# Optimization experiments

Hardware: AMD Instinct MI355X
Metric: run time of the kernel (lower is better)

Reference implementation:

```python
import jax, jax.numpy as jnp
import numpy as np

B, S, D, H, HD, NF, NL, V = 16, 2048, 768, 12, 64, 32, 12, 2362
EPS = 1e-6  # fast_transformers LinearAttention eps


def _rope_tables(seq_len, dim):
    inv_freq = 1.0 / (10000.0 ** (jnp.arange(0, dim, 2, dtype=jnp.float32) / dim))
    t = jnp.arange(seq_len, dtype=jnp.float32)
    freqs = jnp.einsum('s,f->sf', t, inv_freq)
    emb = jnp.concatenate([freqs, freqs], axis=-1)[None, :, None, :]  # [1,S,1,HD]
    return jnp.cos(emb), jnp.sin(emb)


def _rot_half(x):
    x1, x2 = jnp.split(x, 2, axis=-1)
    return jnp.concatenate([-x2, x1], axis=-1)


def _ln(x, g, b):
    m = jnp.mean(x, axis=-1, keepdims=True)
    v = jnp.var(x, axis=-1, keepdims=True)
    return (x - m) / jnp.sqrt(v + 1e-5) * g + b


def setup_inputs():
    key = jax.random.key(0)
    ks = jax.random.split(key, 16)
    w = lambda k, shape: jax.random.normal(k, shape, jnp.float32) * 0.02
    return {
        'idx': jax.random.randint(ks[0], (B, S), 0, V),
        'mask': jnp.ones((B, S), jnp.int32),
        'emb': w(ks[1], (V, D)),
        'wq': w(ks[2], (NL, D, D)), 'bq': jnp.zeros((NL, D), jnp.float32),
        'wk': w(ks[3], (NL, D, D)), 'bk': jnp.zeros((NL, D), jnp.float32),
        'wv': w(ks[4], (NL, D, D)), 'bv': jnp.zeros((NL, D), jnp.float32),
        'wo': w(ks[5], (NL, D, D)), 'bo': jnp.zeros((NL, D), jnp.float32),
        'omega': jax.random.normal(ks[6], (NL, HD, NF), jnp.float32),
        'g1': jnp.ones((NL, D), jnp.float32), 'be1': jnp.zeros((NL, D), jnp.float32),
        'w1': w(ks[7], (NL, D, D)), 'c1': jnp.zeros((NL, D), jnp.float32),
        'w2': w(ks[8], (NL, D, D)), 'c2': jnp.zeros((NL, D), jnp.float32),
        'g2': jnp.ones((NL, D), jnp.float32), 'be2': jnp.zeros((NL, D), jnp.float32),
        'gf': jnp.ones((D,), jnp.float32), 'bf': jnp.zeros((D,), jnp.float32),
    }


def reference(idx, mask, emb, wq, bq, wk, bk, wv, bv, wo, bo, omega,
              g1, be1, w1, c1, w2, c2, g2, be2, gf, bf):
    x = emb[idx]                     # token embedding [B,S,D]; dropout = identity (eval)
    m = mask.astype(x.dtype)         # LengthMask from mask.sum(-1); mask is contiguous ones
    cos, sin = _rope_tables(S, HD)
    for l in range(NL):
        q = (x @ wq[l] + bq[l]).reshape(B, S, H, HD)
        k = (x @ wk[l] + bk[l]).reshape(B, S, H, HD)
        v = (x @ wv[l] + bv[l]).reshape(B, S, H, HD)
        q = q * cos + _rot_half(q) * sin
        k = k * cos + _rot_half(k) * sin
        # GeneralizedRandomFeatures: phi(x) = relu(x @ omega)
        Qf = jax.nn.relu(jnp.einsum('bshd,df->bshf', q, omega[l]))
        Kf = jax.nn.relu(jnp.einsum('bshd,df->bshf', k, omega[l])) * m[:, :, None, None]
        KV = jnp.einsum('bshf,bshd->bhfd', Kf, v)                       # [B,H,NF,HD]
        Z = 1.0 / (jnp.einsum('bshf,bhf->bsh', Qf, Kf.sum(axis=1)) + EPS)
        a = jnp.einsum('bshf,bhfd,bsh->bshd', Qf, KV, Z).reshape(B, S, D)
        x = x + (a @ wo[l] + bo[l])           # residual (dropout=identity)
        x = _ln(x, g1[l], be1[l])             # post-norm
        y = jax.nn.gelu(x @ w1[l] + c1[l], approximate=False) @ w2[l] + c2[l]
        x = _ln(x + y, g2[l], be2[l])
    return _ln(x, gf, bf)                     # final encoder LayerNorm
```

## Files before the change

### kernel.cpp

```cpp
#include <hip/hip_runtime.h>
#include <cstdint>
#include <cstddef>

typedef __bf16 bf16;
typedef __bf16 bf16x8 __attribute__((ext_vector_type(8)));
typedef __bf16 bf16x4 __attribute__((ext_vector_type(4)));
typedef float f32x4 __attribute__((ext_vector_type(4)));

#define NB 16
#define SS 2048
#define HH 12
#define NLL 12
#define MTOK (NB*SS)

#define BARRIER() do { asm volatile("" ::: "memory"); __builtin_amdgcn_s_barrier(); asm volatile("" ::: "memory"); } while (0)
#define VMCNT0()  asm volatile("s_waitcnt vmcnt(0)" ::: "memory")

__device__ __forceinline__ void load16_lds(const bf16* g, bf16* l) {
    __builtin_amdgcn_global_load_lds((const __attribute__((address_space(1))) void*)g,
                                     (__attribute__((address_space(3))) void*)l, 16, 0, 0);
}

__global__ void diag_k(float* out, float code) {
    if (threadIdx.x == 0 && blockIdx.x == 0) out[0] = code;
}

__global__ __launch_bounds__(256) void packw_k(const float* __restrict__ wq, const float* __restrict__ wk,
                                               const float* __restrict__ wv, const float* __restrict__ wo,
                                               const float* __restrict__ w1, const float* __restrict__ w2,
                                               int l, bf16* qkvT_l, bf16* oT_l, bf16* w1T_l, bf16* w2T_l) {
    __shared__ float tile[32][33];
    int which = blockIdx.z;
    const float* srcs[6] = {wq, wk, wv, wo, w1, w2};
    const float* src = srcs[which] + (size_t)l * 589824;
    bf16* dst;
    if (which < 3)       dst = qkvT_l + (size_t)which * 589824;
    else if (which == 3) dst = oT_l;
    else if (which == 4) dst = w1T_l;
    else                 dst = w2T_l;
    int tx = threadIdx.x, ty = threadIdx.y;
    int bx = blockIdx.x, by = blockIdx.y;
#pragma unroll
    for (int j = 0; j < 4; ++j)
        tile[ty + j*8][tx] = src[(size_t)(by*32 + ty + j*8) * 768 + bx*32 + tx];
    __syncthreads();
#pragma unroll
    for (int j = 0; j < 4; ++j)
        dst[(size_t)(bx*32 + ty + j*8) * 768 + by*32 + tx] = (bf16)tile[tx][ty + j*8];
}

__global__ void packb_k(const float* __restrict__ bq, const float* __restrict__ bk,
                        const float* __restrict__ bv, float* bqkv) {
    int i = blockIdx.x * 256 + threadIdx.x;
    if (i >= NLL * 2304) return;
    int l = i / 2304, c = i % 2304;
    float v = (c < 768) ? bq[l*768 + c] : (c < 1536) ? bk[l*768 + c - 768] : bv[l*768 + c - 1536];
    bqkv[i] = v;
}

__global__ void rope_k(float* cosT, float* sinT) {
    int i = blockIdx.x * 256 + threadIdx.x;
    int s = i >> 6, j = i & 63, f = j & 31;
    float inv = powf(10000.f, -(float)(2*f) * (1.0f/64.0f));
    float ang = (float)s * inv;
    cosT[i] = cosf(ang);
    sinT[i] = sinf(ang);
}

__global__ __launch_bounds__(192) void embed_k(const int* __restrict__ idx, const float* __restrict__ emb,
                                               float* __restrict__ x, bf16* __restrict__ xb) {
    size_t tok = blockIdx.x;
    int t = threadIdx.x;
    int id = idx[tok];
    float4 v = *(const float4*)&emb[(size_t)id * 768 + t*4];
    *(float4*)&x[tok * 768 + t*4] = v;
    bf16x4 o; o[0] = (bf16)v.x; o[1] = (bf16)v.y; o[2] = (bf16)v.z; o[3] = (bf16)v.w;
    *(bf16x4*)&xb[tok * 768 + t*4] = o;
}

__global__ __launch_bounds__(512, 2)
void gemm256_k(const bf16* __restrict__ A, const bf16* __restrict__ Bt,
               const float* __restrict__ bias, bf16* __restrict__ outb, int N) {
    const int K = 768;
    __shared__ bf16 As[2][16384];
    __shared__ bf16 Bs[2][16384];
    const int t = threadIdx.x;
    const int w = t >> 6, lane = t & 63;
    const int wr = w >> 2, wc = w & 3;

    const int nx = gridDim.x;
    const int L = blockIdx.y * nx + blockIdx.x;
    const int xcd = L & 7, bi = L >> 3;
    const int bcol = (bi % nx) * 256;
    const int brow = ((bi / nx) * 8 + xcd) * 256;

    const int srow0 = t >> 3;
    const int scb   = (t & 7) * 16;
    const int scbs  = scb ^ ((srow0 & 7) << 4);
    const int scol  = scbs >> 1;

    auto stageA = [&](int s, int k0, int hh) {
        const bf16* g0 = A + (size_t)(brow + hh*128 + srow0)      * K + k0 + scol;
        const bf16* g1 = A + (size_t)(brow + hh*128 + srow0 + 64) * K + k0 + scol;
        load16_lds(g0, &As[s][hh*8192 + t*8]);
        load16_lds(g1, &As[s][hh*8192 + t*8 + 4096]);
    };
    auto stageB = [&](int s, int k0, int hh) {
        const bf16* g0 = Bt + (size_t)(bcol + hh*128 + srow0)      * K + k0 + scol;
        const bf16* g1 = Bt + (size_t)(bcol + hh*128 + srow0 + 64) * K + k0 + scol;
        load16_lds(g0, &Bs[s][hh*8192 + t*8]);
        load16_lds(g1, &Bs[s][hh*8192 + t*8 + 4096]);
    };

    const int rowa = lane & 15, kg = lane >> 4;
    const int rsw  = (rowa & 7) << 4;

    f32x4  acc[8][4] = {};
    bf16x8 af[4][2];
    bf16x8 bg[2][2][2];

#define LOADAF(CUR, MH)                                                          \
    _Pragma("unroll") for (int mi2 = 0; mi2 < 4; ++mi2)                          \
    _Pragma("unroll") for (int ks = 0; ks < 2; ++ks) {                           \
        int lrow = wr*128 + (MH)*64 + mi2*16 + rowa;                             \
        int cbyt = (ks*64 + kg*16) ^ rsw;                                        \
        af[mi2][ks] = *(const bf16x8*)&As[CUR][lrow*64 + (cbyt >> 1)];           \
    }
#define LOADBG(CUR, NH)                                                          \
    _Pragma("unroll") for (int ni2 = 0; ni2 < 2; ++ni2)                          \
    _Pragma("unroll") for (int ks = 0; ks < 2; ++ks) {                           \
        int lrow = wc*64 + (NH)*32 + ni2*16 + rowa;                              \
        int cbyt = (ks*64 + kg*16) ^ rsw;                                        \
        bg[NH][ni2][ks] = *(const bf16x8*)&Bs[CUR][lrow*64 + (cbyt >> 1)];       \
    }
#define MFMAQ(MH, NH)                                                            \
    __builtin_amdgcn_s_setprio(1);                                               \
    _Pragma("unroll") for (int mi2 = 0; mi2 < 4; ++mi2)                          \
    _Pragma("unroll") for (int ni2 = 0; ni2 < 2; ++ni2)                          \
    _Pragma("unroll") for (int ks = 0; ks < 2; ++ks)                             \
        acc[(MH)*4+mi2][(NH)*2+ni2] = __builtin_amdgcn_mfma_f32_16x16x32_bf16(   \
            af[mi2][ks], bg[NH][ni2][ks], acc[(MH)*4+mi2][(NH)*2+ni2], 0, 0, 0); \
    __builtin_amdgcn_s_setprio(0);

    stageA(0, 0, 0); stageA(0, 0, 1); stageB(0, 0, 0); stageB(0, 0, 1);
    VMCNT0();
    BARRIER();

    for (int kt = 0; kt < 12; ++kt) {
        const int cur = kt & 1, nb = cur ^ 1;
        const int kn = (kt + 1) * 64;
        const bool st = (kt < 11);
        LOADAF(cur, 0);
        LOADBG(cur, 0);
        if (st) { stageA(nb, kn, 0); stageA(nb, kn, 1); }
        BARRIER();
        MFMAQ(0, 0);
        BARRIER();
        LOADBG(cur, 1);
        if (st) stageB(nb, kn, 0);
        BARRIER();
        MFMAQ(0, 1);
        BARRIER();
        LOADAF(cur, 1);
        if (st) stageB(nb, kn, 1);
        BARRIER();
        MFMAQ(1, 1);
        BARRIER();
        MFMAQ(1, 0);
        VMCNT0();
        BARRIER();
    }
#undef LOADAF
#undef LOADBG
#undef MFMAQ

    bf16* Cs = &As[0][0];
    const int r0 = (lane >> 4) * 4, c0 = lane & 15;
    const int ch = t & 15, rr = t >> 4;
#pragma unroll
    for (int h = 0; h < 2; ++h) {
        __syncthreads();
        if ((wc >> 1) == h) {
            const int lc0 = (wc & 1) * 64;
#pragma unroll
            for (int mi = 0; mi < 8; ++mi)
#pragma unroll
                for (int ni = 0; ni < 4; ++ni) {
                    int col = bcol + wc * 64 + ni * 16 + c0;
                    float bv = bias[col];
#pragma unroll
                    for (int r = 0; r < 4; ++r)
                        Cs[(wr*128 + mi*16 + r0 + r) * 128 + lc0 + ni*16 + c0] =
                            (bf16)(acc[mi][ni][r] + bv);
                }
        }
        __syncthreads();
#pragma unroll
        for (int i = 0; i < 8; ++i) {
            int row = rr + i * 32;
            *(bf16x8*)&outb[(size_t)(brow + row) * N + bcol + h*128 + ch*8] =
                *(const bf16x8*)&Cs[row * 128 + ch * 8];
        }
    }
}

template <int MODE>
__global__ __launch_bounds__(256)
void gemm128_k(const bf16* __restrict__ A, const bf16* __restrict__ Bt,
               const float* __restrict__ bias, bf16* __restrict__ outb, int N) {
    const int K = 768;
    __shared__ bf16 sh[16384];
    bf16* As = sh;
    bf16* Bs = sh + 8192;
    const int t = threadIdx.x;
    const int w = t >> 6, lane = t & 63;
    const int wr = w >> 1, wc = w & 1;

    const int nx = gridDim.x;
    const int L = blockIdx.y * nx + blockIdx.x;
    const int xcd = L & 7, bi = L >> 3;
    const int bcol = (bi % nx) * 128;
    const int brow = ((bi / nx) * 8 + xcd) * 128;

    const int srow = t >> 3;
    const int scol = (((t & 7) * 16) ^ ((srow & 7) << 4)) >> 1;
    const int rowa = lane & 15, kg = lane >> 4;
    const int rsw  = (rowa & 7) << 4;

    f32x4 acc[4][4] = {};

    for (int k0 = 0; k0 < K; k0 += 64) {
        __syncthreads();
#pragma unroll
        for (int j = 0; j < 4; ++j) {
            load16_lds(A  + (size_t)(brow + j*32 + srow) * K + k0 + scol, &As[j*2048 + t*8]);
            load16_lds(Bt + (size_t)(bcol + j*32 + srow) * K + k0 + scol, &Bs[j*2048 + t*8]);
        }
        __syncthreads();
        bf16x8 af[4][2], bg[4][2];
#pragma unroll
        for (int mi = 0; mi < 4; ++mi)
#pragma unroll
            for (int ks = 0; ks < 2; ++ks)
                af[mi][ks] = *(const bf16x8*)&As[(wr*64 + mi*16 + rowa)*64 + (((ks*64 + kg*16) ^ rsw) >> 1)];
#pragma unroll
        for (int ni = 0; ni < 4; ++ni)
#pragma unroll
            for (int ks = 0; ks < 2; ++ks)
                bg[ni][ks] = *(const bf16x8*)&Bs[(wc*64 + ni*16 + rowa)*64 + (((ks*64 + kg*16) ^ rsw) >> 1)];
#pragma unroll
        for (int mi = 0; mi < 4; ++mi)
#pragma unroll
            for (int ni = 0; ni < 4; ++ni)
#pragma unroll
                for (int ks = 0; ks < 2; ++ks)
                    acc[mi][ni] = __builtin_amdgcn_mfma_f32_16x16x32_bf16(af[mi][ks], bg[ni][ks], acc[mi][ni], 0, 0, 0);
    }

    __syncthreads();
    const int r0 = (lane >> 4) * 4, c0 = lane & 15;
#pragma unroll
    for (int mi = 0; mi < 4; ++mi)
#pragma unroll
        for (int ni = 0; ni < 4; ++ni) {
            int col = bcol + wc * 64 + ni * 16 + c0;
            float bv = bias[col];
#pragma unroll
            for (int r = 0; r < 4; ++r) {
                float v = acc[mi][ni][r] + bv;
                if (MODE == 1) v = 0.5f * v * (1.f + erff(v * 0.70710678118f));
                sh[(wr*64 + mi*16 + r0 + r) * 128 + wc*64 + ni*16 + c0] = (bf16)v;
            }
        }
    __syncthreads();
    const int ch = t & 15, rr = t >> 4;
#pragma unroll
    for (int i = 0; i < 8; ++i) {
        int row = rr + i * 16;
        *(bf16x8*)&outb[(size_t)(brow + row) * N + bcol + ch*8] =
            *(const bf16x8*)&sh[row * 128 + ch * 8];
    }
}

__global__ __launch_bounds__(192) void phi_k(const bf16* __restrict__ qkv, const float* __restrict__ cosT,
                                             const float* __restrict__ sinT, const float* __restrict__ omega_l,
                                             const int* __restrict__ mask, bf16* __restrict__ Qf,
                                             bf16* __restrict__ Kf) {
    __shared__ float roped[2][4][12][65];
    __shared__ float om[64][32];
    int t = threadIdx.x;
    size_t tok0 = (size_t)blockIdx.x * 4;

    for (int i = t; i < 2048; i += 192) ((float*)om)[i] = omega_l[i];

    {
        int side = t / 96, cr = t % 96, h = cr >> 3, cq = cr & 7;
        float sgn = (cq < 4) ? -1.f : 1.f;
        for (int it = 0; it < 4; ++it) {
            size_t tokg = tok0 + it;
            int s = (int)(tokg & (SS - 1));
            const bf16* rowp = qkv + tokg * 2304 + side * 768 + h * 64;
            bf16x8 mv = *(const bf16x8*)(rowp + cq * 8);
            bf16x8 pv = *(const bf16x8*)(rowp + (cq ^ 4) * 8);
            const float* cp = cosT + s * 64 + cq * 8;
            const float* sp = sinT + s * 64 + cq * 8;
#pragma unroll
            for (int e = 0; e < 8; ++e) {
                float r = (float)mv[e] * cp[e] + sgn * (float)pv[e] * sp[e];
                roped[side][it][h][cq * 8 + e] = r;
            }
        }
    }
    __syncthreads();

    int side = t / 96, rr = t % 96, h = rr >> 3, f0 = (rr & 7) * 4;
    float acc[4][4] = {};
    for (int d = 0; d < 64; ++d) {
        float4 o = *(const float4*)&om[d][f0];
#pragma unroll
        for (int tk = 0; tk < 4; ++tk) {
            float qv = roped[side][tk][h][d];
            acc[tk][0] += qv * o.x; acc[tk][1] += qv * o.y;
            acc[tk][2] += qv * o.z; acc[tk][3] += qv * o.w;
        }
    }
    bf16* outb = (side == 0) ? Qf : Kf;
#pragma unroll
    for (int tk = 0; tk < 4; ++tk) {
        size_t tokg = tok0 + tk;
        float m = (side == 1) ? (float)mask[tokg] : 1.f;
        bf16x4 v;
        v[0] = (bf16)(fmaxf(acc[tk][0], 0.f) * m);
        v[1] = (bf16)(fmaxf(acc[tk][1], 0.f) * m);
        v[2] = (bf16)(fmaxf(acc[tk][2], 0.f) * m);
        v[3] = (bf16)(fmaxf(acc[tk][3], 0.f) * m);
        *(bf16x4*)&outb[(tokg * 12 + h) * 32 + f0] = v;
    }
}

__global__ __launch_bounds__(256) void kvp_k(const bf16* __restrict__ Kf, const bf16* __restrict__ qkv,
                                             float* __restrict__ KVp, float* __restrict__ Ksp) {
    int ch = blockIdx.x, h = blockIdx.y, b = blockIdx.z;
    __shared__ float kts[64][32];
    __shared__ bf16 vts[64][64];
    int t = threadIdx.x;
    int fg = t & 15, dg = t >> 4;
    int f0 = fg * 2, d0 = dg * 4;
    float acc[8] = {};
    float ksm[2] = {};
    for (int s0 = ch * 256; s0 < ch * 256 + 256; s0 += 64) {
        __syncthreads();
        {
            int row = t >> 2, slot = t & 3;
            bf16x8 k8 = *(const bf16x8*)&Kf[((size_t)(b * SS + s0 + row) * 12 + h) * 32 + slot * 8];
#pragma unroll
            for (int e = 0; e < 8; ++e) kts[row][slot * 8 + e] = (float)k8[e];
            int c0 = t, c1 = t + 256;
            *(float4*)&vts[c0 >> 3][(c0 & 7) * 8] =
                *(const float4*)&qkv[(size_t)(b * SS + s0 + (c0 >> 3)) * 2304 + 1536 + h * 64 + (c0 & 7) * 8];
            *(float4*)&vts[c1 >> 3][(c1 & 7) * 8] =
                *(const float4*)&qkv[(size_t)(b * SS + s0 + (c1 >> 3)) * 2304 + 1536 + h * 64 + (c1 & 7) * 8];
        }
        __syncthreads();
#pragma unroll 4
        for (int sl = 0; sl < 64; ++sl) {
            float2 kk = *(const float2*)&kts[sl][f0];
            bf16x4 vv = *(const bf16x4*)&vts[sl][d0];
            float v0 = (float)vv[0], v1 = (float)vv[1], v2 = (float)vv[2], v3 = (float)vv[3];
            acc[0] += kk.x * v0; acc[1] += kk.x * v1; acc[2] += kk.x * v2; acc[3] += kk.x * v3;
            acc[4] += kk.y * v0; acc[5] += kk.y * v1; acc[6] += kk.y * v2; acc[7] += kk.y * v3;
            if (dg == 0) { ksm[0] += kk.x; ksm[1] += kk.y; }
        }
    }
    size_t base = (((size_t)(b * 12 + h) * 8 + ch) * 32) * 64;
#pragma unroll
    for (int i = 0; i < 2; ++i)
#pragma unroll
        for (int j = 0; j < 4; ++j)
            KVp[base + (size_t)(f0 + i) * 64 + d0 + j] = acc[i * 4 + j];
    if (dg == 0) {
        size_t kb = ((size_t)(b * 12 + h) * 8 + ch) * 32;
        Ksp[kb + f0] = ksm[0]; Ksp[kb + f0 + 1] = ksm[1];
    }
}

__global__ __launch_bounds__(256) void kvc_k(const float* __restrict__ KVp, const float* __restrict__ Ksp,
                                             float* __restrict__ KV, float* __restrict__ Ksum) {
    int bh = blockIdx.x, t = threadIdx.x;
    size_t base = (size_t)bh * 8 * 2048;
    float v[8] = {};
    for (int ch = 0; ch < 8; ++ch)
#pragma unroll
        for (int j = 0; j < 8; ++j) v[j] += KVp[base + (size_t)ch * 2048 + t * 8 + j];
#pragma unroll
    for (int j = 0; j < 8; ++j) KV[(size_t)bh * 2048 + t * 8 + j] = v[j];
    if (t < 32) {
        float s = 0.f;
        for (int ch = 0; ch < 8; ++ch) s += Ksp[((size_t)bh * 8 + ch) * 32 + t];
        Ksum[(size_t)bh * 32 + t] = s;
    }
}

__global__ __launch_bounds__(256) void comb_k(const bf16* __restrict__ Qf, const float* __restrict__ KV,
                                              const float* __restrict__ Ksum, bf16* __restrict__ aout) {
    int ch = blockIdx.x, h = blockIdx.y, b = blockIdx.z;
    int bh = b * 12 + h;
    int t = threadIdx.x, sl = t >> 6, d = t & 63;
    const float* kvb = KV + (size_t)bh * 2048;
    const float* ksb = Ksum + (size_t)bh * 32;
    float kvcol[32], ksr[32];
#pragma unroll
    for (int f = 0; f < 32; ++f) kvcol[f] = kvb[f * 64 + d];
#pragma unroll
    for (int f = 0; f < 32; ++f) ksr[f] = ksb[f];
    for (int g = 0; g < 16; ++g) {
        int s = ch * 64 + g * 4 + sl;
        size_t tok = (size_t)b * SS + s;
        const bf16* qf = Qf + (tok * 12 + h) * 32;
        float accd = 0.f, accz = 0.f;
#pragma unroll
        for (int fb = 0; fb < 4; ++fb) {
            bf16x8 q8 = *(const bf16x8*)(qf + fb * 8);
#pragma unroll
            for (int e = 0; e < 8; ++e) {
                float q = (float)q8[e];
                accd += q * kvcol[fb * 8 + e];
                accz += q * ksr[fb * 8 + e];
            }
        }
        float z = 1.f / (accz + 1e-6f);
        aout[tok * 768 + h * 64 + d] = (bf16)(accd * z);
    }
}

__global__ __launch_bounds__(192) void ln2_k(const float* xsrc, const bf16* ysrc,
                                             const float* __restrict__ g, const float* __restrict__ be,
                                             float* xout, bf16* xbout) {
    size_t tok = blockIdx.x;
    int t = threadIdx.x;
    float4 v = *(const float4*)&xsrc[tok * 768 + t * 4];
    if (ysrc) {
        bf16x4 yv = *(const bf16x4*)&ysrc[tok * 768 + t * 4];
        v.x += (float)yv[0]; v.y += (float)yv[1]; v.z += (float)yv[2]; v.w += (float)yv[3];
    }
    float s = v.x + v.y + v.z + v.w;
    float q = v.x * v.x + v.y * v.y + v.z * v.z + v.w * v.w;
#pragma unroll
    for (int off = 32; off > 0; off >>= 1) { s += __shfl_down(s, off); q += __shfl_down(q, off); }
    __shared__ float sred[3], qred[3];
    int w = t >> 6, lane = t & 63;
    if (lane == 0) { sred[w] = s; qred[w] = q; }
    __syncthreads();
    s = sred[0] + sred[1] + sred[2];
    q = qred[0] + qred[1] + qred[2];
    float mean = s * (1.f / 768.f);
    float var = q * (1.f / 768.f) - mean * mean;
    float inv = rsqrtf(var + 1e-5f);
    float4 gg = *(const float4*)&g[t * 4];
    float4 bb = *(const float4*)&be[t * 4];
    float4 o;
    o.x = (v.x - mean) * inv * gg.x + bb.x;
    o.y = (v.y - mean) * inv * gg.y + bb.y;
    o.z = (v.z - mean) * inv * gg.z + bb.z;
    o.w = (v.w - mean) * inv * gg.w + bb.w;
    *(float4*)&xout[tok * 768 + t * 4] = o;
    if (xbout) {
        bf16x4 ob; ob[0] = (bf16)o.x; ob[1] = (bf16)o.y; ob[2] = (bf16)o.z; ob[3] = (bf16)o.w;
        *(bf16x4*)&xbout[tok * 768 + t * 4] = ob;
    }
}

extern "C" void kernel_launch(void* const* d_in, const int* in_sizes, int n_in,
                              void* d_out, int out_size, void* d_ws, size_t ws_size,
                              hipStream_t stream) {
    const int*   idx   = (const int*)d_in[0];
    const int*   mask  = (const int*)d_in[1];
    const float* emb   = (const float*)d_in[2];
    const float* wq    = (const float*)d_in[3];
    const float* bq    = (const float*)d_in[4];
    const float* wk    = (const float*)d_in[5];
    const float* bk    = (const float*)d_in[6];
    const float* wv    = (const float*)d_in[7];
    const float* bv    = (const float*)d_in[8];
    const float* wo    = (const float*)d_in[9];
    const float* bo    = (const float*)d_in[10];
    const float* omega = (const float*)d_in[11];
    const float* g1    = (const float*)d_in[12];
    const float* be1   = (const float*)d_in[13];
    const float* w1    = (const float*)d_in[14];
    const float* c1    = (const float*)d_in[15];
    const float* w2    = (const float*)d_in[16];
    const float* c2    = (const float*)d_in[17];
    const float* g2    = (const float*)d_in[18];
    const float* be2   = (const float*)d_in[19];
    const float* gf    = (const float*)d_in[20];
    const float* bff   = (const float*)d_in[21];
    float* dout = (float*)d_out;

    char* wsb = (char*)d_ws;
    size_t off = 0;
    auto nxt = [&](size_t bytes) -> void* {
        void* p = wsb + off;
        off += bytes;
        off = (off + 255) & ~(size_t)255;
        return p;
    };

    float* cosT  = (float*)nxt((size_t)SS * 64 * 4);
    float* sinT  = (float*)nxt((size_t)SS * 64 * 4);
    bf16*  qkvTl = (bf16*)nxt((size_t)2304 * 768 * 2);
    bf16*  oTl   = (bf16*)nxt((size_t)768 * 768 * 2);
    bf16*  w1Tl  = (bf16*)nxt((size_t)768 * 768 * 2);
    bf16*  w2Tl  = (bf16*)nxt((size_t)768 * 768 * 2);
    float* bqkv  = (float*)nxt((size_t)NLL * 2304 * 4);
    float* x     = (float*)nxt((size_t)MTOK * 768 * 4);
    bf16*  xb    = (bf16*)nxt((size_t)MTOK * 768 * 2);
    bf16*  qkv   = (bf16*)nxt((size_t)MTOK * 2304 * 2);
    bf16*  Qf    = (bf16*)nxt((size_t)MTOK * 384 * 2);
    bf16*  Kf    = (bf16*)nxt((size_t)MTOK * 384 * 2);
    float* KVp   = (float*)nxt((size_t)NB * HH * 8 * 2048 * 4);
    float* Ksp   = (float*)nxt((size_t)NB * HH * 8 * 32 * 4);
    float* KV    = (float*)nxt((size_t)NB * HH * 2048 * 4);
    float* Ksum  = (float*)nxt((size_t)NB * HH * 32 * 4);
    size_t needed = off;

    if (ws_size < needed) {
        diag_k<<<dim3(1), dim3(64), 0, stream>>>(dout, 10000.f + (float)(ws_size >> 20));
        return;
    }

    bf16* abuf = qkv;
    bf16* h1   = (bf16*)((char*)qkv + (size_t)MTOK * 768 * 2);
    bf16* y    = (bf16*)((char*)qkv + (size_t)MTOK * 768 * 4);

    packb_k<<<dim3((NLL * 2304 + 255) / 256), dim3(256), 0, stream>>>(bq, bk, bv, bqkv);
    rope_k<<<dim3(SS * 64 / 256), dim3(256), 0, stream>>>(cosT, sinT);
    embed_k<<<dim3(MTOK), dim3(192), 0, stream>>>(idx, emb, x, xb);

    for (int l = 0; l < NLL; ++l) {
        const float* bqkv_l = bqkv + (size_t)l * 2304;
        const float* om_l   = omega + (size_t)l * 2048;

        packw_k<<<dim3(24, 24, 6), dim3(32, 8), 0, stream>>>(wq, wk, wv, wo, w1, w2, l, qkvTl, oTl, w1Tl, w2Tl);
        gemm256_k<<<dim3(9, 128), dim3(512), 0, stream>>>(xb, qkvTl, bqkv_l, qkv, 2304);
        phi_k<<<dim3(MTOK / 4), dim3(192), 0, stream>>>(qkv, cosT, sinT, om_l, mask, Qf, Kf);
        kvp_k<<<dim3(8, HH, NB), dim3(256), 0, stream>>>(Kf, qkv, KVp, Ksp);
        kvc_k<<<dim3(NB * HH), dim3(256), 0, stream>>>(KVp, Ksp, KV, Ksum);
        comb_k<<<dim3(32, HH, NB), dim3(256), 0, stream>>>(Qf, KV, Ksum, abuf);
        gemm128_k<0><<<dim3(6, 256), dim3(256), 0, stream>>>(abuf, oTl, bo + (size_t)l * 768, y, 768);
        ln2_k<<<dim3(MTOK), dim3(192), 0, stream>>>(x, y, g1 + (size_t)l * 768, be1 + (size_t)l * 768, x, xb);
        gemm128_k<1><<<dim3(6, 256), dim3(256), 0, stream>>>(xb, w1Tl, c1 + (size_t)l * 768, h1, 768);
        gemm128_k<0><<<dim3(6, 256), dim3(256), 0, stream>>>(h1, w2Tl, c2 + (size_t)l * 768, y, 768);
        ln2_k<<<dim3(MTOK), dim3(192), 0, stream>>>(x, y, g2 + (size_t)l * 768, be2 + (size_t)l * 768, x, xb);
    }
    ln2_k<<<dim3(MTOK), dim3(192), 0, stream>>>(x, nullptr, gf, bff, dout, nullptr);
}
```

Before: 7.265 ms.

## Deepen QKV GEMM prefetch by splitting LDS stages into quarter-tile loads

Restructures the QKV projection GEMM's global-to-LDS staging so each K tile is loaded in quarter pieces matched to the MFMA sub-block order. Pieces for tile k+2 are issued into the current buffer as soon as that part has been consumed. The per-iteration full vmcnt(0) wait becomes a partial wait of six outstanding loads, and the loop is fully unrolled. This aims to hide global load latency better. In exchange it depends on exact ordering of LDS reuse and outstanding-load counts, so a subtle race is possible.

```diff
diff --git a/kernel.cpp b/kernel.cpp
--- a/kernel.cpp
+++ b/kernel.cpp
@@ -14,7 +14,7 @@
 #define MTOK (NB*SS)
 
 #define BARRIER() do { asm volatile("" ::: "memory"); __builtin_amdgcn_s_barrier(); asm volatile("" ::: "memory"); } while (0)
-#define VMCNT0()  asm volatile("s_waitcnt vmcnt(0)" ::: "memory")
+#define VMCNTN(N) asm volatile("s_waitcnt vmcnt(" #N ")" ::: "memory")
 
 __device__ __forceinline__ void load16_lds(const bf16* g, bf16* l) {
     __builtin_amdgcn_global_load_lds((const __attribute__((address_space(1))) void*)g,
@@ -79,8 +79,8 @@
 }
 
 __global__ __launch_bounds__(512, 2)
-void gemm256_k(const bf16* __restrict__ A, const bf16* __restrict__ Bt,
-               const float* __restrict__ bias, bf16* __restrict__ outb, int N) {
+void gemm256p_k(const bf16* __restrict__ A, const bf16* __restrict__ Bt,
+                const float* __restrict__ bias, bf16* __restrict__ outb, int N) {
     const int K = 768;
     __shared__ bf16 As[2][16384];
     __shared__ bf16 Bs[2][16384];
@@ -95,21 +95,25 @@
     const int brow = ((bi / nx) * 8 + xcd) * 256;
 
     const int srow0 = t >> 3;
-    const int scb   = (t & 7) * 16;
-    const int scbs  = scb ^ ((srow0 & 7) << 4);
-    const int scol  = scbs >> 1;
-
-    auto stageA = [&](int s, int k0, int hh) {
-        const bf16* g0 = A + (size_t)(brow + hh*128 + srow0)      * K + k0 + scol;
-        const bf16* g1 = A + (size_t)(brow + hh*128 + srow0 + 64) * K + k0 + scol;
-        load16_lds(g0, &As[s][hh*8192 + t*8]);
-        load16_lds(g1, &As[s][hh*8192 + t*8 + 4096]);
+    const int cc    = (t & 7) * 8;
+    const int scol  = (((t & 7) * 16) ^ ((srow0 & 7) << 4)) >> 1;
+    const int brow0b = srow0 + (srow0 & 32);
+
+    auto stA_MH0 = [&](int bf, int k0) {
+        load16_lds(A + (size_t)(brow +   0 + srow0) * K + k0 + scol, &As[bf][t*8]);
+        load16_lds(A + (size_t)(brow + 128 + srow0) * K + k0 + scol, &As[bf][t*8 + 8192]);
     };
-    auto stageB = [&](int s, int k0, int hh) {
-        const bf16* g0 = Bt + (size_t)(bcol + hh*128 + srow0)      * K + k0 + scol;
-        const bf16* g1 = Bt + (size_t)(bcol + hh*128 + srow0 + 64) * K + k0 + scol;
-        load16_lds(g0, &Bs[s][hh*8192 + t*8]);
-        load16_lds(g1, &Bs[s][hh*8192 + t*8 + 4096]);
+    auto stA_MH1 = [&](int bf, int k0) {
+        load16_lds(A + (size_t)(brow +  64 + srow0) * K + k0 + scol, &As[bf][t*8 + 4096]);
+        load16_lds(A + (size_t)(brow + 192 + srow0) * K + k0 + scol, &As[bf][t*8 + 12288]);
+    };
+    auto stB_n0 = [&](int bf, int k0) {
+        load16_lds(Bt + (size_t)(bcol + brow0b      ) * K + k0 + scol, &Bs[bf][brow0b*64 + cc]);
+        load16_lds(Bt + (size_t)(bcol + brow0b + 128) * K + k0 + scol, &Bs[bf][brow0b*64 + cc + 8192]);
+    };
+    auto stB_n1 = [&](int bf, int k0) {
+        load16_lds(Bt + (size_t)(bcol + brow0b +  32) * K + k0 + scol, &Bs[bf][(brow0b+32)*64 + cc]);
+        load16_lds(Bt + (size_t)(bcol + brow0b + 160) * K + k0 + scol, &Bs[bf][(brow0b+32)*64 + cc + 8192]);
     };
 
     const int rowa = lane & 15, kg = lane >> 4;
@@ -142,32 +146,35 @@
             af[mi2][ks], bg[NH][ni2][ks], acc[(MH)*4+mi2][(NH)*2+ni2], 0, 0, 0); \
     __builtin_amdgcn_s_setprio(0);
 
-    stageA(0, 0, 0); stageA(0, 0, 1); stageB(0, 0, 0); stageB(0, 0, 1);
-    VMCNT0();
+    stA_MH0(0, 0); stA_MH1(0, 0); stB_n0(0, 0); stB_n1(0, 0);
+    stA_MH0(1, 64); stB_n0(1, 64); stB_n1(1, 64);
+    VMCNTN(6);
     BARRIER();
 
+#pragma unroll
     for (int kt = 0; kt < 12; ++kt) {
         const int cur = kt & 1, nb = cur ^ 1;
-        const int kn = (kt + 1) * 64;
-        const bool st = (kt < 11);
+        const int kn1 = (kt + 1) * 64, kn2 = (kt + 2) * 64;
         LOADAF(cur, 0);
         LOADBG(cur, 0);
-        if (st) { stageA(nb, kn, 0); stageA(nb, kn, 1); }
+        if (kt < 11) stA_MH1(nb, kn1);
         BARRIER();
         MFMAQ(0, 0);
         BARRIER();
         LOADBG(cur, 1);
-        if (st) stageB(nb, kn, 0);
+        if (kt < 10) stA_MH0(cur, kn2);
         BARRIER();
         MFMAQ(0, 1);
         BARRIER();
         LOADAF(cur, 1);
-        if (st) stageB(nb, kn, 1);
+        if (kt < 10) stB_n0(cur, kn2);
         BARRIER();
         MFMAQ(1, 1);
         BARRIER();
+        if (kt < 10) stB_n1(cur, kn2);
         MFMAQ(1, 0);
-        VMCNT0();
+        if (kt <= 9)       { VMCNTN(6); }
+        else if (kt == 10) { VMCNTN(0); }
         BARRIER();
     }
 #undef LOADAF
@@ -542,7 +549,7 @@
         const float* om_l   = omega + (size_t)l * 2048;
 
         packw_k<<<dim3(24, 24, 6), dim3(32, 8), 0, stream>>>(wq, wk, wv, wo, w1, w2, l, qkvTl, oTl, w1Tl, w2Tl);
-        gemm256_k<<<dim3(9, 128), dim3(512), 0, stream>>>(xb, qkvTl, bqkv_l, qkv, 2304);
+        gemm256p_k<<<dim3(9, 128), dim3(512), 0, stream>>>(xb, qkvTl, bqkv_l, qkv, 2304);
         phi_k<<<dim3(MTOK / 4), dim3(192), 0, stream>>>(qkv, cosT, sinT, om_l, mask, Qf, Kf);
         kvp_k<<<dim3(8, HH, NB), dim3(256), 0, stream>>>(Kf, qkv, KVp, Ksp);
         kvc_k<<<dim3(NB * HH), dim3(256), 0, stream>>>(KVp, Ksp, KV, Ksum);
```

Result: slower. 7.436 ms (+2.4%).
